# Kernel tuning notes

Measured on AMD Instinct MI355X. Metric: run time of the kernel, lower is better.

## Reference

```python
import jax, jax.numpy as jnp
import numpy as np
import math

B, L, D, H, R = 2, 1024, 768, 12, 256
DH = D // H  # 64


def layernorm(x, g, b, eps=1e-5):
    mu = jnp.mean(x, axis=-1, keepdims=True)
    var = jnp.mean((x - mu) ** 2, axis=-1, keepdims=True)
    return (x - mu) / jnp.sqrt(var + eps) * g + b


def setup_inputs() -> dict:
    key = jax.random.key(0)
    ks = jax.random.split(key, 8)
    x = jax.random.normal(ks[0], (B, L, D), dtype=jnp.float32)
    conv_w = jax.random.normal(ks[1], (D, 3), dtype=jnp.float32) * 0.3   # depthwise k=3
    conv_b = jnp.zeros((D,), jnp.float32)
    ln_g = jnp.ones((D,), jnp.float32)
    ln_b = jnp.zeros((D,), jnp.float32)
    qkv_w = jax.random.normal(ks[2], (3 * D, D), dtype=jnp.float32) / math.sqrt(D)
    qkv_b = jnp.zeros((3 * D,), jnp.float32)
    bn_w1 = jax.random.normal(ks[3], (R, D), dtype=jnp.float32) / math.sqrt(D)
    bn_w2 = jax.random.normal(ks[4], (H * 5, R), dtype=jnp.float32) / math.sqrt(R)
    temperature = jnp.ones((1,), jnp.float32) * 0.5
    proj_w = jax.random.normal(ks[5], (D, D), dtype=jnp.float32) / math.sqrt(D)
    proj_b = jnp.zeros((D,), jnp.float32)
    mn_g = jnp.ones((DH,), jnp.float32)
    mn_b = jnp.zeros((DH,), jnp.float32)
    return {"x": x, "conv_w": conv_w, "conv_b": conv_b, "ln_g": ln_g, "ln_b": ln_b,
            "qkv_w": qkv_w, "qkv_b": qkv_b, "bn_w1": bn_w1, "bn_w2": bn_w2,
            "temperature": temperature, "proj_w": proj_w, "proj_b": proj_b,
            "mn_g": mn_g, "mn_b": mn_b}


def reference(x, conv_w, conv_b, ln_g, ln_b, qkv_w, qkv_b, bn_w1, bn_w2,
              temperature, proj_w, proj_b, mn_g, mn_b):
    Bx, Lx, Dx = x.shape
    # causal depthwise conv1d (kernel 3, pad 2 then drop last 2 == left-pad 2)
    xp = jnp.pad(x, ((0, 0), (2, 0), (0, 0)))
    conv = (xp[:, 0:Lx] * conv_w[:, 0] + xp[:, 1:Lx + 1] * conv_w[:, 1]
            + xp[:, 2:Lx + 2] * conv_w[:, 2]) + conv_b
    x_conv = x + conv
    xn = layernorm(x_conv, ln_g, ln_b)

    qkv = xn @ qkv_w.T + qkv_b
    q, k, v = jnp.split(qkv, 3, axis=-1)

    params = (jax.nn.silu(xn @ bn_w1.T) @ bn_w2.T).reshape(Bx, Lx, H, 5)
    sem_amp = jax.nn.sigmoid(params[..., 0])
    sem_phase = jnp.tanh(params[..., 1]) * math.pi
    ctx_amp = jax.nn.sigmoid(params[..., 2])
    ctx_phase = jnp.tanh(params[..., 3]) * math.pi
    decay = 0.3 + 0.65 * jax.nn.sigmoid(params[..., 4])  # (B,L,H)
    gate = jax.nn.sigmoid(sem_amp * ctx_amp * jnp.cos(sem_phase - ctx_phase) * temperature[0])

    q_f = (jax.nn.elu(q) + 1.0).reshape(Bx, Lx, H, DH)
    k_f = (jax.nn.elu(k) + 1.0).reshape(Bx, Lx, H, DH)
    v_f = v.reshape(Bx, Lx, H, DH)

    one_minus = 1.0 - decay                                    # (B,L,H)
    kv_input = jnp.einsum('blhd,blhe->blhde', k_f, v_f)        # (B,L,H,dh,dh)
    kv_input = jnp.clip(kv_input * (gate * one_minus)[..., None, None], -5.0, 5.0)

    df = jnp.exp(jnp.cumsum(jnp.log(decay), axis=1))           # (B,L,H)
    safe_df = df + 1e-8
    kv_states = jnp.cumsum(kv_input / safe_df[..., None, None], axis=1) * df[..., None, None]

    z = jnp.cumsum(k_f * one_minus[..., None] / safe_df[..., None], axis=1) * df[..., None]
    z = jnp.clip(z, -10000.0, 10000.0)

    out_num = jnp.einsum('blhd,blhde->blhe', q_f, kv_states)   # (B,L,H,dh)
    den = jnp.sum(q_f * z, axis=-1, keepdims=True) + 0.0001
    out = layernorm(out_num / den, mn_g, mn_b)                 # (B,L,H,dh)

    y = out.reshape(Bx, Lx, Dx) @ proj_w.T + proj_b
    return y, gate
```

## Files before the change

### kernel.cpp

```cpp
#include <hip/hip_runtime.h>
#include <math.h>

#define LL 1024
#define DD 768
#define HH 12
#define CL 16
#define NC 64
#define NBH 24

typedef __bf16 bf16x8 __attribute__((ext_vector_type(8)));
typedef __bf16 bf16x4 __attribute__((ext_vector_type(4)));
typedef float floatx4 __attribute__((ext_vector_type(4)));

typedef const void __attribute__((address_space(1)))* gas_ptr;
typedef void __attribute__((address_space(3)))* las_ptr;

__device__ __forceinline__ void gl_lds16(const void* g, void* s) {
  __builtin_amdgcn_global_load_lds((gas_ptr)g, (las_ptr)s, 16, 0, 0);
}

__device__ __forceinline__ float wave_sum64(float v) {
#pragma unroll
  for (int off = 32; off; off >>= 1) v += __shfl_xor(v, off, 64);
  return v;
}

__device__ __forceinline__ float sigm(float x) { return 1.0f / (1.0f + expf(-x)); }
__device__ __forceinline__ float clamp5(float x) {
  return __builtin_amdgcn_fmed3f(x, -5.f, 5.f);
}

__global__ __launch_bounds__(256) void prep_kernel(
    const float* __restrict__ x, const float* __restrict__ cw,
    const float* __restrict__ cb, const float* __restrict__ g,
    const float* __restrict__ bta, __bf16* __restrict__ xn,
    const float* __restrict__ qkvw, const float* __restrict__ bnw1,
    const float* __restrict__ projw, const float* __restrict__ w2,
    __bf16* __restrict__ wqb, __bf16* __restrict__ dp, __bf16* __restrict__ dw2) {
  if (blockIdx.x >= 2048) {
    int i = (blockIdx.x - 2048) * 256 + threadIdx.x;
    if (i >= 647168) return;
    bf16x4 o;
    if (i >= 638976) {
      int off = i - 638976;
      if (off < 3840) {
        float4 v = ((const float4*)w2)[off];
        o[0] = (__bf16)v.x; o[1] = (__bf16)v.y; o[2] = (__bf16)v.z; o[3] = (__bf16)v.w;
      } else {
        o[0] = (__bf16)0.f; o[1] = (__bf16)0.f; o[2] = (__bf16)0.f; o[3] = (__bf16)0.f;
      }
      ((bf16x4*)dw2)[off] = o;
      return;
    }
    const float* s; __bf16* d; int off;
    if (i < 442368)      { s = qkvw;  d = wqb;  off = i; }
    else if (i < 491520) { s = bnw1;  d = wqb;  off = i; }
    else                 { s = projw; d = dp;   off = i - 491520; }
    int soff = (i < 442368) ? i : (i < 491520 ? i - 442368 : off);
    float4 v = ((const float4*)s)[soff];
    o[0] = (__bf16)v.x; o[1] = (__bf16)v.y; o[2] = (__bf16)v.z; o[3] = (__bf16)v.w;
    ((bf16x4*)d)[off] = o;
    return;
  }
  int row = blockIdx.x;
  int l = row & (LL - 1);
  const float* xr = x + (size_t)row * DD;
  __shared__ float red[16];
  float vals[3];
  float s = 0.f, ss = 0.f;
#pragma unroll
  for (int i = 0; i < 3; i++) {
    int d = threadIdx.x + i * 256;
    float x0 = xr[d];
    float xm1 = (l >= 1) ? xr[d - DD] : 0.f;
    float xm2 = (l >= 2) ? xr[d - 2 * DD] : 0.f;
    float c = xm2 * cw[d * 3 + 0] + xm1 * cw[d * 3 + 1] + x0 * cw[d * 3 + 2] + cb[d];
    float v = x0 + c;
    vals[i] = v; s += v; ss += v * v;
  }
  s = wave_sum64(s); ss = wave_sum64(ss);
  int wid = threadIdx.x >> 6;
  if ((threadIdx.x & 63) == 0) { red[wid * 2] = s; red[wid * 2 + 1] = ss; }
  __syncthreads();
  if (threadIdx.x == 0) {
    red[8] = red[0] + red[2] + red[4] + red[6];
    red[9] = red[1] + red[3] + red[5] + red[7];
  }
  __syncthreads();
  float mu = red[8] * (1.f / 768.f);
  float var = red[9] * (1.f / 768.f) - mu * mu;
  float inv = rsqrtf(var + 1e-5f);
  __bf16* xo = xn + (size_t)row * DD;
#pragma unroll
  for (int i = 0; i < 3; i++) {
    int d = threadIdx.x + i * 256;
    xo[d] = (__bf16)((vals[i] - mu) * inv * g[d] + bta[d]);
  }
}

template <int BM, int NY, int MODE, bool HASBIAS, bool OUTBF>
__global__ __launch_bounds__(256) void gemm_mfma_kernel(
    const __bf16* __restrict__ A, const __bf16* __restrict__ Bw,
    const float* __restrict__ bias, void* __restrict__ Cv, void* __restrict__ C2,
    int M, int N, int K) {
  constexpr int MI = BM / 32;
  constexpr int NYG = NY / 8;
  __shared__ __attribute__((aligned(16))) __bf16 As[BM * 64];
  __shared__ __attribute__((aligned(16))) __bf16 Bs[128 * 64];
  int id = blockIdx.x;
  int by = (id & 7) * NYG + ((id >> 3) % NYG);
  int bx = (id >> 3) / NYG;
  int m0 = by * BM, n0 = bx * 128;
  int tid = threadIdx.x;
  int w = tid >> 6, lane = tid & 63;
  int wm = w >> 1, wn = w & 1;
  int quad = lane >> 4, l16 = lane & 15;

  int lrow = lane >> 3;
  int lchunk = (lane & 7) ^ lrow;
  int R0 = w * 8;

  floatx4 acc[MI][4];
#pragma unroll
  for (int i = 0; i < MI; i++)
#pragma unroll
    for (int j = 0; j < 4; j++) acc[i][j] = (floatx4)0.f;

  for (int k0 = 0; k0 < K; k0 += 64) {
    __syncthreads();
#pragma unroll
    for (int r = 0; r < BM / 32; r++) {
      int row = r * 32 + R0 + lrow;
      gl_lds16(A + (size_t)(m0 + row) * K + k0 + lchunk * 8, &As[(r * 32 + R0) * 64]);
    }
#pragma unroll
    for (int r = 0; r < 4; r++) {
      int row = r * 32 + R0 + lrow;
      gl_lds16(Bw + (size_t)(n0 + row) * K + k0 + lchunk * 8, &Bs[(r * 32 + R0) * 64]);
    }
    __syncthreads();
#pragma unroll
    for (int s = 0; s < 2; s++) {
      bf16x8 af[MI], bfr[4];
      int csw = (s << 2) + quad;
#pragma unroll
      for (int i = 0; i < MI; i++) {
        int m = wm * (BM / 2) + i * 16 + l16;
        af[i] = *(const bf16x8*)&As[m * 64 + (csw ^ (l16 & 7)) * 8];
      }
#pragma unroll
      for (int j = 0; j < 4; j++) {
        int n = wn * 64 + j * 16 + l16;
        bfr[j] = *(const bf16x8*)&Bs[n * 64 + (csw ^ (l16 & 7)) * 8];
      }
#pragma unroll
      for (int i = 0; i < MI; i++)
#pragma unroll
        for (int j = 0; j < 4; j++)
          acc[i][j] = __builtin_amdgcn_mfma_f32_16x16x32_bf16(af[i], bfr[j], acc[i][j], 0, 0, 0);
    }
  }
#pragma unroll
  for (int j = 0; j < 4; j++) {
    int gcol = n0 + wn * 64 + j * 16 + l16;
    if (MODE == 3) {
      if (gcol < 2304) {
        float bv = bias[gcol];
        bool isqk = gcol < 1536;
#pragma unroll
        for (int i = 0; i < MI; i++) {
          int grow = m0 + wm * (BM / 2) + i * 16 + quad * 4;
#pragma unroll
          for (int r = 0; r < 4; r++) {
            float v = acc[i][j][r] + bv;
            if (isqk) v = (v > 0.f) ? v + 1.f : expf(v);
            ((__bf16*)Cv)[(size_t)(grow + r) * 2304 + gcol] = (__bf16)v;
          }
        }
      } else {
        int hcol = gcol - 2304;
#pragma unroll
        for (int i = 0; i < MI; i++) {
          int grow = m0 + wm * (BM / 2) + i * 16 + quad * 4;
#pragma unroll
          for (int r = 0; r < 4; r++) {
            float v = acc[i][j][r];
            v = v / (1.f + expf(-v));
            ((__bf16*)C2)[(size_t)(grow + r) * 256 + hcol] = (__bf16)v;
          }
        }
      }
    } else {
      float bv = HASBIAS ? bias[gcol] : 0.f;
#pragma unroll
      for (int i = 0; i < MI; i++) {
        int grow = m0 + wm * (BM / 2) + i * 16 + quad * 4;
#pragma unroll
        for (int r = 0; r < 4; r++) {
          float v = acc[i][j][r] + bv;
          if (OUTBF) ((__bf16*)Cv)[(size_t)(grow + r) * N + gcol] = (__bf16)v;
          else       ((float*)Cv)[(size_t)(grow + r) * N + gcol] = v;
        }
      }
    }
  }
}

__global__ __launch_bounds__(256) void params_df_kernel(
    const float* __restrict__ pp, const float* __restrict__ temp,
    float* __restrict__ gate, float* __restrict__ dec, float* __restrict__ dfb) {
  int bh = blockIdx.x;
  int b = bh / HH, h = bh - b * HH;
  int tid = threadIdx.x;
  int lane = tid & 63, wid = tid >> 6;
  float tv = temp[0];
  const float PI = 3.14159265358979323846f;
  double ls[4];
  double lsum = 0.0;
#pragma unroll
  for (int i = 0; i < 4; i++) {
    int l = tid * 4 + i;
    int row = (b << 10) + l;
    const float* p = pp + (size_t)row * 128 + h * 5;
    float p0 = p[0], p1 = p[1], p2 = p[2], p3 = p[3], p4 = p[4];
    float sa = sigm(p0);
    float sp = tanhf(p1) * PI;
    float ca = sigm(p2);
    float cp = tanhf(p3) * PI;
    float dc = 0.3f + 0.65f * sigm(p4);
    float gt = sigm(sa * ca * cosf(sp - cp) * tv);
    gate[row * HH + h] = gt;
    dec[(bh << 10) + l] = dc;
    lsum += (double)logf(dc);
    ls[i] = lsum;
  }
  double run = lsum;
#pragma unroll
  for (int off = 1; off < 64; off <<= 1) {
    double n = __shfl_up(run, off, 64);
    if (lane >= off) run += n;
  }
  __shared__ double wsum[4];
  if (lane == 63) wsum[wid] = run;
  __syncthreads();
  double wexcl = 0.0;
  for (int k = 0; k < wid; k++) wexcl += wsum[k];
  double excl = wexcl + run - lsum;
  float* dfo = dfb + (bh << 10) + tid * 4;
#pragma unroll
  for (int i = 0; i < 4; i++) dfo[i] = expf((float)(excl + ls[i]));
}

__global__ __launch_bounds__(256, 6) void scan_phase1(
    const __bf16* __restrict__ qkv, const float* __restrict__ dec,
    const float* __restrict__ df, const float* __restrict__ gate,
    __bf16* __restrict__ kvcs, float* __restrict__ zcs, float* __restrict__ Aarr) {
  int blk = blockIdx.x;
  int bh = blk >> 6, c = blk & (NC - 1);
  int b = bh / HH, h = bh - b * HH;
  int tid = threadIdx.x;
  int w = tid >> 6, e = tid & 63;
  int t0 = c * CL;
  __shared__ __attribute__((aligned(16))) __bf16 kbuf[CL][64];
  __shared__ __attribute__((aligned(16))) __bf16 vbuf[CL][64];
  __shared__ float sbuf[CL][4];
  {
    int trow = ((w & 1) << 3) + (e >> 3);
    int chunk = e & 7;
    int sec = (w < 2) ? 1 : 2;
    const __bf16* gp = qkv + ((size_t)(b * LL + t0 + trow) * 2304 + sec * 768 + h * 64 + chunk * 8);
    void* dst = (w < 2) ? (void*)&kbuf[(w & 1) << 3][0] : (void*)&vbuf[(w & 1) << 3][0];
    gl_lds16(gp, dst);
  }
  if (tid < CL) {
    int t = t0 + tid;
    float a = dec[bh * LL + t];
    float d = df[bh * LL + t];
    float r = d / (d + 1e-8f);
    float g = gate[(b * LL + t) * HH + h];
    sbuf[tid][0] = a; sbuf[tid][1] = r; sbuf[tid][2] = g * (1.f - a);
    sbuf[tid][3] = (1.f - a) * r;
  }
  __syncthreads();
  float KV[16];
#pragma unroll
  for (int d = 0; d < 16; d++) KV[d] = 0.f;
  float z = 0.f, A = 1.f;
  for (int t = 0; t < CL; t++) {
    float a = sbuf[t][0], r = sbuf[t][1], cs = sbuf[t][2], w1r = sbuf[t][3];
    float vc = (float)vbuf[t][e] * cs;
    A *= a;
    bf16x8 k0 = *(const bf16x8*)&kbuf[t][w << 4];
    bf16x8 k1 = *(const bf16x8*)&kbuf[t][(w << 4) + 8];
#pragma unroll
    for (int j = 0; j < 8; j++) {
      float u = clamp5((float)k0[j] * vc);
      KV[j] = fmaf(a, KV[j], r * u);
    }
#pragma unroll
    for (int j = 0; j < 8; j++) {
      float u = clamp5((float)k1[j] * vc);
      KV[8 + j] = fmaf(a, KV[8 + j], r * u);
    }
    z = fmaf(a, z, (float)kbuf[t][e] * w1r);
  }
  __bf16* kvo = kvcs + (size_t)blk * 4096 + (w << 4) * 64 + e;
#pragma unroll
  for (int d = 0; d < 16; d++) kvo[d * 64] = (__bf16)KV[d];
  if (w == 0) zcs[blk * 64 + e] = z;
  if (tid == 0) Aarr[blk] = A;
}

__global__ __launch_bounds__(256) void combine_kernel(
    const float* __restrict__ Aarr, __bf16* __restrict__ kv, float* __restrict__ z) {
  int g = blockIdx.x * 256 + threadIdx.x;
  if (g < NBH * 4096) {
    int bh = g >> 12, idx = g & 4095;
    const float* Ap = Aarr + bh * NC;
    __bf16* p = kv + (size_t)bh * NC * 4096 + idx;
    float carry = 0.f;
#pragma unroll 8
    for (int c = 0; c < NC; c++) {
      float endv = (float)p[(size_t)c * 4096];
      p[(size_t)c * 4096] = (__bf16)carry;
      carry = fmaf(Ap[c], carry, endv);
    }
  } else {
    int g2 = g - NBH * 4096;
    if (g2 >= NBH * 64) return;
    int bh = g2 >> 6, idx = g2 & 63;
    const float* Ap = Aarr + bh * NC;
    float* p = z + bh * NC * 64 + idx;
    float carry = 0.f;
#pragma unroll 8
    for (int c = 0; c < NC; c++) {
      float endv = p[c * 64];
      p[c * 64] = carry;
      carry = fmaf(Ap[c], carry, endv);
    }
  }
}

__global__ __launch_bounds__(256, 6) void scan_phase3(
    const __bf16* __restrict__ qkv, const float* __restrict__ dec,
    const float* __restrict__ df, const float* __restrict__ gate,
    const __bf16* __restrict__ kvcs, const float* __restrict__ zcs,
    const float* __restrict__ mng, const float* __restrict__ mnb,
    __bf16* __restrict__ att) {
  int blk = blockIdx.x;
  int bh = blk >> 6, c = blk & (NC - 1);
  int b = bh / HH, h = bh - b * HH;
  int tid = threadIdx.x;
  int w = tid >> 6, e = tid & 63;
  int t0 = c * CL;
  __shared__ __attribute__((aligned(16))) __bf16 qbuf[CL][64];
  __shared__ __attribute__((aligned(16))) __bf16 kbuf[CL][64];
  __shared__ __attribute__((aligned(16))) __bf16 vbuf[CL][64];
  __shared__ float sbuf[CL][4];
  __shared__ float pbuf[8][4][64];
  {
    int trow = ((w & 1) << 3) + (e >> 3);
    int chunk = e & 7;
    size_t rowbase = (size_t)(b * LL + t0 + trow) * 2304 + h * 64 + chunk * 8;
    if (w < 2) {
      gl_lds16(qkv + rowbase, &qbuf[(w & 1) << 3][0]);
      gl_lds16(qkv + rowbase + 768, &kbuf[(w & 1) << 3][0]);
    } else {
      gl_lds16(qkv + rowbase + 1536, &vbuf[(w & 1) << 3][0]);
    }
  }
  if (tid < CL) {
    int t = t0 + tid;
    float a = dec[bh * LL + t];
    float d = df[bh * LL + t];
    float r = d / (d + 1e-8f);
    float g = gate[(b * LL + t) * HH + h];
    sbuf[tid][0] = a; sbuf[tid][1] = r; sbuf[tid][2] = g * (1.f - a);
    sbuf[tid][3] = (1.f - a) * r;
  }
  float KV[16];
  const __bf16* kvi = kvcs + (size_t)blk * 4096 + (w << 4) * 64 + e;
#pragma unroll
  for (int d = 0; d < 16; d++) KV[d] = (float)kvi[d * 64];
  float z = zcs[blk * 64 + e];
  float zsnap[4];
  float mg = mng[e], mb = mnb[e];
  __syncthreads();
#pragma unroll
  for (int half = 0; half < 2; half++) {
    for (int tt = 0; tt < 8; tt++) {
      int t = (half << 3) + tt;
      float a = sbuf[t][0], r = sbuf[t][1], cs = sbuf[t][2], w1r = sbuf[t][3];
      float vc = (float)vbuf[t][e] * cs;
      float onp = 0.f;
      bf16x8 k0 = *(const bf16x8*)&kbuf[t][w << 4];
      bf16x8 k1 = *(const bf16x8*)&kbuf[t][(w << 4) + 8];
      bf16x8 q0 = *(const bf16x8*)&qbuf[t][w << 4];
      bf16x8 q1 = *(const bf16x8*)&qbuf[t][(w << 4) + 8];
#pragma unroll
      for (int j = 0; j < 8; j++) {
        float u = clamp5((float)k0[j] * vc);
        float nv = fmaf(a, KV[j], r * u);
        KV[j] = nv;
        onp = fmaf((float)q0[j], nv, onp);
      }
#pragma unroll
      for (int j = 0; j < 8; j++) {
        float u = clamp5((float)k1[j] * vc);
        float nv = fmaf(a, KV[8 + j], r * u);
        KV[8 + j] = nv;
        onp = fmaf((float)q1[j], nv, onp);
      }
      pbuf[tt][w][e] = onp;
      z = fmaf(a, z, (float)kbuf[t][e] * w1r);
      if ((tt >> 1) == w) zsnap[(half << 1) | (tt & 1)] = z;
    }
    __syncthreads();
#pragma unroll
    for (int i = 0; i < 2; i++) {
      int tt = (w << 1) + i;
      int t = (half << 3) + tt;
      float on = pbuf[tt][0][e] + pbuf[tt][1][e] + pbuf[tt][2][e] + pbuf[tt][3][e];
      float zc = __builtin_amdgcn_fmed3f(zsnap[(half << 1) | i], -10000.f, 10000.f);
      float qe = (float)qbuf[t][e];
      float s0 = qe * zc, s1 = on, s2 = on * on;
#pragma unroll
      for (int off = 32; off; off >>= 1) {
        s0 += __shfl_xor(s0, off, 64);
        s1 += __shfl_xor(s1, off, 64);
        s2 += __shfl_xor(s2, off, 64);
      }
      float den = s0 + 1e-4f;
      float idn = 1.f / den;
      float o = on * idn;
      float mu = s1 * idn * (1.f / 64.f);
      float E2 = s2 * idn * idn * (1.f / 64.f);
      float var = E2 - mu * mu;
      float outv = (o - mu) * rsqrtf(var + 1e-5f) * mg + mb;
      att[((size_t)(b * LL + t0 + t)) * DD + h * 64 + e] = (__bf16)outv;
    }
    if (half == 0) __syncthreads();
  }
}

extern "C" void kernel_launch(void* const* d_in, const int* in_sizes, int n_in,
                              void* d_out, int out_size, void* d_ws, size_t ws_size,
                              hipStream_t stream) {
  (void)in_sizes; (void)n_in; (void)out_size; (void)ws_size;
  const float* x           = (const float*)d_in[0];
  const float* conv_w      = (const float*)d_in[1];
  const float* conv_b      = (const float*)d_in[2];
  const float* ln_g        = (const float*)d_in[3];
  const float* ln_b        = (const float*)d_in[4];
  const float* qkv_w       = (const float*)d_in[5];
  const float* qkv_b       = (const float*)d_in[6];
  const float* bn_w1       = (const float*)d_in[7];
  const float* bn_w2       = (const float*)d_in[8];
  const float* temperature = (const float*)d_in[9];
  const float* proj_w      = (const float*)d_in[10];
  const float* proj_b      = (const float*)d_in[11];
  const float* mn_g        = (const float*)d_in[12];
  const float* mn_b        = (const float*)d_in[13];

  float* y    = (float*)d_out;
  float* gate = y + 2 * 1024 * 768;

  char* ws = (char*)d_ws;
  __bf16* xn_bf   = (__bf16*)(ws);
  __bf16* att_bf  = xn_bf;
  __bf16* qkva    = (__bf16*)(ws + 3145728);
  __bf16* hbuf_bf = (__bf16*)(ws + 12582912);
  float*  pp      = (float*)(ws + 13631488);
  float*  dec     = (float*)(ws + 14680064);
  float*  dfb     = (float*)(ws + 14778368);
  __bf16* kvcs    = (__bf16*)(ws + 14876672);
  __bf16* wqb_bf  = (__bf16*)(ws + 14876672);
  float*  zcs     = (float*)(ws + 27459584);
  float*  Aarr    = (float*)(ws + 27852800);
  __bf16* projw_bf= (__bf16*)(ws + 27858944);
  __bf16* w2p_bf  = (__bf16*)(ws + 29038592);

  prep_kernel<<<4576, 256, 0, stream>>>(x, conv_w, conv_b, ln_g, ln_b, xn_bf,
                                        qkv_w, bn_w1, proj_w, bn_w2,
                                        wqb_bf, projw_bf, w2p_bf);

  gemm_mfma_kernel<64, 32, 3, true, false><<<640, 256, 0, stream>>>(
      xn_bf, wqb_bf, qkv_b, qkva, hbuf_bf, 2048, 2560, 768);

  gemm_mfma_kernel<64, 32, 0, false, false><<<32, 256, 0, stream>>>(
      hbuf_bf, w2p_bf, nullptr, pp, nullptr, 2048, 128, 256);

  params_df_kernel<<<NBH, 256, 0, stream>>>(pp, temperature, gate, dec, dfb);

  scan_phase1<<<NBH * NC, 256, 0, stream>>>(qkva, dec, dfb, gate, kvcs, zcs, Aarr);

  combine_kernel<<<390, 256, 0, stream>>>(Aarr, kvcs, zcs);

  scan_phase3<<<NBH * NC, 256, 0, stream>>>(qkva, dec, dfb, gate, kvcs, zcs,
                                            mn_g, mn_b, att_bf);

  gemm_mfma_kernel<64, 32, 0, true, false><<<192, 256, 0, stream>>>(
      att_bf, projw_bf, proj_b, y, nullptr, 2048, 768, 768);
}
```

Before: 180.0 us.

## Compute intra-chunk scan outputs in phase1 and make phase3 a carry-correction pass

Phase1 now also computes the intra-chunk output numerators, the local z values and the per-step decay prefix products, and writes them to workspace. Phase3 no longer re-runs the recurrence. It applies the inter-chunk carry as q·KV_carry scaled by the prefix product, adds the stored local partials, then does the normalisation with 16-lane reductions and vectorised stores. This removes the duplicated scan work in phase3, at the cost of extra global traffic for the outp and zloc buffers, which are large fp32 arrays. The GEMM grid mapping is also simplified from a swizzled 1D index to a plain 2D grid, which may change L2 locality.

Result: faster. 173.9 us (-3.3%).

```diff
diff --git a/kernel.cpp b/kernel.cpp
--- a/kernel.cpp
+++ b/kernel.cpp
@@ -52,11 +52,10 @@
       ((bf16x4*)dw2)[off] = o;
       return;
     }
-    const float* s; __bf16* d; int off;
-    if (i < 442368)      { s = qkvw;  d = wqb;  off = i; }
-    else if (i < 491520) { s = bnw1;  d = wqb;  off = i; }
-    else                 { s = projw; d = dp;   off = i - 491520; }
-    int soff = (i < 442368) ? i : (i < 491520 ? i - 442368 : off);
+    const float* s; __bf16* d; int off, soff;
+    if (i < 442368)      { s = qkvw;  d = wqb; off = i; soff = i; }
+    else if (i < 491520) { s = bnw1;  d = wqb; off = i; soff = i - 442368; }
+    else                 { s = projw; d = dp;  off = i - 491520; soff = off; }
     float4 v = ((const float4*)s)[soff];
     o[0] = (__bf16)v.x; o[1] = (__bf16)v.y; o[2] = (__bf16)v.z; o[3] = (__bf16)v.w;
     ((bf16x4*)d)[off] = o;
@@ -98,24 +97,19 @@
   }
 }
 
-template <int BM, int NY, int MODE, bool HASBIAS, bool OUTBF>
+template <int BM, int MODE, bool HASBIAS, bool OUTBF>
 __global__ __launch_bounds__(256) void gemm_mfma_kernel(
     const __bf16* __restrict__ A, const __bf16* __restrict__ Bw,
     const float* __restrict__ bias, void* __restrict__ Cv, void* __restrict__ C2,
     int M, int N, int K) {
   constexpr int MI = BM / 32;
-  constexpr int NYG = NY / 8;
   __shared__ __attribute__((aligned(16))) __bf16 As[BM * 64];
   __shared__ __attribute__((aligned(16))) __bf16 Bs[128 * 64];
-  int id = blockIdx.x;
-  int by = (id & 7) * NYG + ((id >> 3) % NYG);
-  int bx = (id >> 3) / NYG;
-  int m0 = by * BM, n0 = bx * 128;
+  int m0 = blockIdx.y * BM, n0 = blockIdx.x * 128;
   int tid = threadIdx.x;
   int w = tid >> 6, lane = tid & 63;
   int wm = w >> 1, wn = w & 1;
   int quad = lane >> 4, l16 = lane & 15;
-
   int lrow = lane >> 3;
   int lchunk = (lane & 7) ^ lrow;
   int R0 = w * 8;
@@ -254,23 +248,28 @@
 __global__ __launch_bounds__(256, 6) void scan_phase1(
     const __bf16* __restrict__ qkv, const float* __restrict__ dec,
     const float* __restrict__ df, const float* __restrict__ gate,
-    __bf16* __restrict__ kvcs, float* __restrict__ zcs, float* __restrict__ Aarr) {
+    __bf16* __restrict__ kvcs, float* __restrict__ zcs, float* __restrict__ Aarr,
+    float* __restrict__ outp, float* __restrict__ zloc, float* __restrict__ pLoc) {
   int blk = blockIdx.x;
   int bh = blk >> 6, c = blk & (NC - 1);
   int b = bh / HH, h = bh - b * HH;
   int tid = threadIdx.x;
   int w = tid >> 6, e = tid & 63;
   int t0 = c * CL;
+  __shared__ __attribute__((aligned(16))) __bf16 qbuf[CL][64];
   __shared__ __attribute__((aligned(16))) __bf16 kbuf[CL][64];
   __shared__ __attribute__((aligned(16))) __bf16 vbuf[CL][64];
   __shared__ float sbuf[CL][4];
   {
     int trow = ((w & 1) << 3) + (e >> 3);
     int chunk = e & 7;
-    int sec = (w < 2) ? 1 : 2;
-    const __bf16* gp = qkv + ((size_t)(b * LL + t0 + trow) * 2304 + sec * 768 + h * 64 + chunk * 8);
-    void* dst = (w < 2) ? (void*)&kbuf[(w & 1) << 3][0] : (void*)&vbuf[(w & 1) << 3][0];
-    gl_lds16(gp, dst);
+    size_t rowbase = (size_t)(b * LL + t0 + trow) * 2304 + h * 64 + chunk * 8;
+    if (w < 2) {
+      gl_lds16(qkv + rowbase, &qbuf[(w & 1) << 3][0]);
+      gl_lds16(qkv + rowbase + 768, &kbuf[(w & 1) << 3][0]);
+    } else {
+      gl_lds16(qkv + rowbase + 1536, &vbuf[(w & 1) << 3][0]);
+    }
   }
   if (tid < CL) {
     int t = t0 + tid;
@@ -282,33 +281,46 @@
     sbuf[tid][3] = (1.f - a) * r;
   }
   __syncthreads();
+  if (tid == 0) {
+    float run = 1.f;
+#pragma unroll
+    for (int t = 0; t < CL; t++) { run *= sbuf[t][0]; pLoc[blk * 16 + t] = run; }
+    Aarr[blk] = run;
+  }
   float KV[16];
 #pragma unroll
   for (int d = 0; d < 16; d++) KV[d] = 0.f;
-  float z = 0.f, A = 1.f;
+  float z = 0.f;
   for (int t = 0; t < CL; t++) {
     float a = sbuf[t][0], r = sbuf[t][1], cs = sbuf[t][2], w1r = sbuf[t][3];
     float vc = (float)vbuf[t][e] * cs;
-    A *= a;
+    float onp = 0.f;
     bf16x8 k0 = *(const bf16x8*)&kbuf[t][w << 4];
     bf16x8 k1 = *(const bf16x8*)&kbuf[t][(w << 4) + 8];
+    bf16x8 q0 = *(const bf16x8*)&qbuf[t][w << 4];
+    bf16x8 q1 = *(const bf16x8*)&qbuf[t][(w << 4) + 8];
 #pragma unroll
     for (int j = 0; j < 8; j++) {
       float u = clamp5((float)k0[j] * vc);
-      KV[j] = fmaf(a, KV[j], r * u);
+      float nv = fmaf(a, KV[j], r * u);
+      KV[j] = nv;
+      onp = fmaf((float)q0[j], nv, onp);
     }
 #pragma unroll
     for (int j = 0; j < 8; j++) {
       float u = clamp5((float)k1[j] * vc);
-      KV[8 + j] = fmaf(a, KV[8 + j], r * u);
+      float nv = fmaf(a, KV[8 + j], r * u);
+      KV[8 + j] = nv;
+      onp = fmaf((float)q1[j], nv, onp);
     }
     z = fmaf(a, z, (float)kbuf[t][e] * w1r);
+    outp[(size_t)blk * 4096 + t * 256 + (w << 6) + e] = onp;
+    if ((t >> 2) == w) zloc[(size_t)blk * 1024 + t * 64 + e] = z;
   }
   __bf16* kvo = kvcs + (size_t)blk * 4096 + (w << 4) * 64 + e;
 #pragma unroll
   for (int d = 0; d < 16; d++) kvo[d * 64] = (__bf16)KV[d];
   if (w == 0) zcs[blk * 64 + e] = z;
-  if (tid == 0) Aarr[blk] = A;
 }
 
 __global__ __launch_bounds__(256) void combine_kernel(
@@ -341,10 +353,10 @@
   }
 }
 
-__global__ __launch_bounds__(256, 6) void scan_phase3(
-    const __bf16* __restrict__ qkv, const float* __restrict__ dec,
-    const float* __restrict__ df, const float* __restrict__ gate,
-    const __bf16* __restrict__ kvcs, const float* __restrict__ zcs,
+__global__ __launch_bounds__(256) void scan_phase3(
+    const __bf16* __restrict__ qkv, const __bf16* __restrict__ kvcs,
+    const float* __restrict__ zcs, const float* __restrict__ outp,
+    const float* __restrict__ zloc, const float* __restrict__ pLoc,
     const float* __restrict__ mng, const float* __restrict__ mnb,
     __bf16* __restrict__ att) {
   int blk = blockIdx.x;
@@ -354,93 +366,79 @@
   int w = tid >> 6, e = tid & 63;
   int t0 = c * CL;
   __shared__ __attribute__((aligned(16))) __bf16 qbuf[CL][64];
-  __shared__ __attribute__((aligned(16))) __bf16 kbuf[CL][64];
-  __shared__ __attribute__((aligned(16))) __bf16 vbuf[CL][64];
-  __shared__ float sbuf[CL][4];
-  __shared__ float pbuf[8][4][64];
-  {
+  __shared__ __attribute__((aligned(16))) __bf16 kvbuf[64][64];
+  if (w < 2) {
     int trow = ((w & 1) << 3) + (e >> 3);
     int chunk = e & 7;
-    size_t rowbase = (size_t)(b * LL + t0 + trow) * 2304 + h * 64 + chunk * 8;
-    if (w < 2) {
-      gl_lds16(qkv + rowbase, &qbuf[(w & 1) << 3][0]);
-      gl_lds16(qkv + rowbase + 768, &kbuf[(w & 1) << 3][0]);
-    } else {
-      gl_lds16(qkv + rowbase + 1536, &vbuf[(w & 1) << 3][0]);
-    }
-  }
-  if (tid < CL) {
-    int t = t0 + tid;
-    float a = dec[bh * LL + t];
-    float d = df[bh * LL + t];
-    float r = d / (d + 1e-8f);
-    float g = gate[(b * LL + t) * HH + h];
-    sbuf[tid][0] = a; sbuf[tid][1] = r; sbuf[tid][2] = g * (1.f - a);
-    sbuf[tid][3] = (1.f - a) * r;
-  }
-  float KV[16];
-  const __bf16* kvi = kvcs + (size_t)blk * 4096 + (w << 4) * 64 + e;
-#pragma unroll
-  for (int d = 0; d < 16; d++) KV[d] = (float)kvi[d * 64];
-  float z = zcs[blk * 64 + e];
-  float zsnap[4];
-  float mg = mng[e], mb = mnb[e];
+    gl_lds16(qkv + (size_t)(b * LL + t0 + trow) * 2304 + h * 64 + chunk * 8,
+             &qbuf[(w & 1) << 3][0]);
+  }
+#pragma unroll
+  for (int j = 0; j < 2; j++) {
+    int m = (w << 1) | j;
+    gl_lds16(kvcs + (size_t)blk * 4096 + m * 512 + e * 8, &kvbuf[m * 8][0]);
+  }
+  int t = tid >> 4;
+  int e0 = (tid & 15) << 2;
+  float P = pLoc[blk * 16 + t];
+  float4 zi = *(const float4*)&zcs[blk * 64 + e0];
+  float4 zl = *(const float4*)&zloc[(size_t)blk * 1024 + t * 64 + e0];
+  float osum[4] = {0.f, 0.f, 0.f, 0.f};
+#pragma unroll
+  for (int ww = 0; ww < 4; ww++) {
+    float4 o = *(const float4*)&outp[(size_t)blk * 4096 + t * 256 + ww * 64 + e0];
+    osum[0] += o.x; osum[1] += o.y; osum[2] += o.z; osum[3] += o.w;
+  }
+  float4 mg = *(const float4*)&mng[e0];
+  float4 mb = *(const float4*)&mnb[e0];
   __syncthreads();
-#pragma unroll
-  for (int half = 0; half < 2; half++) {
-    for (int tt = 0; tt < 8; tt++) {
-      int t = (half << 3) + tt;
-      float a = sbuf[t][0], r = sbuf[t][1], cs = sbuf[t][2], w1r = sbuf[t][3];
-      float vc = (float)vbuf[t][e] * cs;
-      float onp = 0.f;
-      bf16x8 k0 = *(const bf16x8*)&kbuf[t][w << 4];
-      bf16x8 k1 = *(const bf16x8*)&kbuf[t][(w << 4) + 8];
-      bf16x8 q0 = *(const bf16x8*)&qbuf[t][w << 4];
-      bf16x8 q1 = *(const bf16x8*)&qbuf[t][(w << 4) + 8];
-#pragma unroll
-      for (int j = 0; j < 8; j++) {
-        float u = clamp5((float)k0[j] * vc);
-        float nv = fmaf(a, KV[j], r * u);
-        KV[j] = nv;
-        onp = fmaf((float)q0[j], nv, onp);
-      }
-#pragma unroll
-      for (int j = 0; j < 8; j++) {
-        float u = clamp5((float)k1[j] * vc);
-        float nv = fmaf(a, KV[8 + j], r * u);
-        KV[8 + j] = nv;
-        onp = fmaf((float)q1[j], nv, onp);
-      }
-      pbuf[tt][w][e] = onp;
-      z = fmaf(a, z, (float)kbuf[t][e] * w1r);
-      if ((tt >> 1) == w) zsnap[(half << 1) | (tt & 1)] = z;
-    }
-    __syncthreads();
-#pragma unroll
-    for (int i = 0; i < 2; i++) {
-      int tt = (w << 1) + i;
-      int t = (half << 3) + tt;
-      float on = pbuf[tt][0][e] + pbuf[tt][1][e] + pbuf[tt][2][e] + pbuf[tt][3][e];
-      float zc = __builtin_amdgcn_fmed3f(zsnap[(half << 1) | i], -10000.f, 10000.f);
-      float qe = (float)qbuf[t][e];
-      float s0 = qe * zc, s1 = on, s2 = on * on;
-#pragma unroll
-      for (int off = 32; off; off >>= 1) {
-        s0 += __shfl_xor(s0, off, 64);
-        s1 += __shfl_xor(s1, off, 64);
-        s2 += __shfl_xor(s2, off, 64);
-      }
-      float den = s0 + 1e-4f;
-      float idn = 1.f / den;
-      float o = on * idn;
-      float mu = s1 * idn * (1.f / 64.f);
-      float E2 = s2 * idn * idn * (1.f / 64.f);
-      float var = E2 - mu * mu;
-      float outv = (o - mu) * rsqrtf(var + 1e-5f) * mg + mb;
-      att[((size_t)(b * LL + t0 + t)) * DD + h * 64 + e] = (__bf16)outv;
-    }
-    if (half == 0) __syncthreads();
-  }
+  float ic[4] = {0.f, 0.f, 0.f, 0.f};
+#pragma unroll
+  for (int d0 = 0; d0 < 64; d0 += 8) {
+    bf16x8 qv = *(const bf16x8*)&qbuf[t][d0];
+#pragma unroll
+    for (int j = 0; j < 8; j++) {
+      bf16x4 kv = *(const bf16x4*)&kvbuf[d0 + j][e0];
+      float qf = (float)qv[j];
+#pragma unroll
+      for (int x = 0; x < 4; x++) ic[x] = fmaf(qf, (float)kv[x], ic[x]);
+    }
+  }
+  bf16x4 q4 = *(const bf16x4*)&qbuf[t][e0];
+  float onum[4], zt[4];
+  float s0 = 0.f, s1 = 0.f, s2 = 0.f;
+  float zia[4] = {zi.x, zi.y, zi.z, zi.w};
+  float zla[4] = {zl.x, zl.y, zl.z, zl.w};
+#pragma unroll
+  for (int x = 0; x < 4; x++) {
+    onum[x] = fmaf(P, ic[x], osum[x]);
+    float zv = fmaf(P, zia[x], zla[x]);
+    zt[x] = __builtin_amdgcn_fmed3f(zv, -10000.f, 10000.f);
+    s0 = fmaf((float)q4[x], zt[x], s0);
+    s1 += onum[x];
+    s2 = fmaf(onum[x], onum[x], s2);
+  }
+#pragma unroll
+  for (int off = 1; off < 16; off <<= 1) {
+    s0 += __shfl_xor(s0, off, 64);
+    s1 += __shfl_xor(s1, off, 64);
+    s2 += __shfl_xor(s2, off, 64);
+  }
+  float den = s0 + 1e-4f;
+  float idn = 1.f / den;
+  float mu = s1 * idn * (1.f / 64.f);
+  float E2 = s2 * idn * idn * (1.f / 64.f);
+  float var = E2 - mu * mu;
+  float rst = rsqrtf(var + 1e-5f);
+  float mga[4] = {mg.x, mg.y, mg.z, mg.w};
+  float mba[4] = {mb.x, mb.y, mb.z, mb.w};
+  bf16x4 ov;
+#pragma unroll
+  for (int x = 0; x < 4; x++) {
+    float o = onum[x] * idn;
+    ov[x] = (__bf16)((o - mu) * rst * mga[x] + mba[x]);
+  }
+  *(bf16x4*)&att[((size_t)(b * LL + t0 + t)) * DD + h * 64 + e0] = ov;
 }
 
 extern "C" void kernel_launch(void* const* d_in, const int* in_sizes, int n_in,
@@ -479,26 +477,30 @@
   float*  Aarr    = (float*)(ws + 27852800);
   __bf16* projw_bf= (__bf16*)(ws + 27858944);
   __bf16* w2p_bf  = (__bf16*)(ws + 29038592);
+  float*  outp    = (float*)(ws + 29104128);
+  float*  zloc    = (float*)(ws + 54269952);
+  float*  pLoc    = (float*)(ws + 60561408);
 
   prep_kernel<<<4576, 256, 0, stream>>>(x, conv_w, conv_b, ln_g, ln_b, xn_bf,
                                         qkv_w, bn_w1, proj_w, bn_w2,
                                         wqb_bf, projw_bf, w2p_bf);
 
-  gemm_mfma_kernel<64, 32, 3, true, false><<<640, 256, 0, stream>>>(
+  gemm_mfma_kernel<64, 3, true, false><<<dim3(20, 32), 256, 0, stream>>>(
       xn_bf, wqb_bf, qkv_b, qkva, hbuf_bf, 2048, 2560, 768);
 
-  gemm_mfma_kernel<64, 32, 0, false, false><<<32, 256, 0, stream>>>(
+  gemm_mfma_kernel<64, 0, false, false><<<dim3(1, 32), 256, 0, stream>>>(
       hbuf_bf, w2p_bf, nullptr, pp, nullptr, 2048, 128, 256);
 
   params_df_kernel<<<NBH, 256, 0, stream>>>(pp, temperature, gate, dec, dfb);
 
-  scan_phase1<<<NBH * NC, 256, 0, stream>>>(qkva, dec, dfb, gate, kvcs, zcs, Aarr);
+  scan_phase1<<<NBH * NC, 256, 0, stream>>>(qkva, dec, dfb, gate, kvcs, zcs, Aarr,
+                                            outp, zloc, pLoc);
 
   combine_kernel<<<390, 256, 0, stream>>>(Aarr, kvcs, zcs);
 
-  scan_phase3<<<NBH * NC, 256, 0, stream>>>(qkva, dec, dfb, gate, kvcs, zcs,
+  scan_phase3<<<NBH * NC, 256, 0, stream>>>(qkva, kvcs, zcs, outp, zloc, pLoc,
                                             mn_g, mn_b, att_bf);
 
-  gemm_mfma_kernel<64, 32, 0, true, false><<<192, 256, 0, stream>>>(
+  gemm_mfma_kernel<64, 0, true, false><<<dim3(6, 32), 256, 0, stream>>>(
       att_bf, projw_bf, proj_b, y, nullptr, 2048, 768, 768);
 }
```
